# Kernel tuning notes

Measured on AMD Instinct MI355X. Metric: run time of the kernel, lower is better.

## Reference

```python
import jax, jax.numpy as jnp
import numpy as np

B, H, E = 1024, 2048, 1024

def _xavier(key, shape):
    # torch xavier_normal_ on [1, out, in]: std = sqrt(2/(fan_in+fan_out)) over last two dims
    fan_out, fan_in = shape[-2], shape[-1]
    std = (2.0 / (fan_in + fan_out)) ** 0.5
    return jax.random.normal(key, shape, jnp.float32) * std

def setup_inputs() -> dict:
    key = jax.random.key(0)
    ks = jax.random.split(key, 17)
    inp = {
        'x': jax.random.normal(ks[0], (B, E, 1), jnp.float32),
        'c': jax.random.normal(ks[1], (B, H, 1), jnp.float32),
        'h': jax.random.normal(ks[2], (B, H, 1), jnp.float32),
        'W_xi': _xavier(ks[3], (1, H, E)), 'W_hi': _xavier(ks[4], (1, H, H)), 'B_i': _xavier(ks[5], (1, H, 1)),
        'W_xg': _xavier(ks[6], (1, H, E)), 'W_hg': _xavier(ks[7], (1, H, H)), 'B_g': _xavier(ks[8], (1, H, 1)),
        'W_xf': _xavier(ks[9], (1, H, E)), 'W_hf': _xavier(ks[10], (1, H, H)), 'B_f': _xavier(ks[11], (1, H, 1)),
        'W_xo': _xavier(ks[12], (1, H, E)), 'W_ho': _xavier(ks[13], (1, H, H)), 'B_o': _xavier(ks[14], (1, H, 1)),
        'W_hy': _xavier(ks[15], (1, E, H)), 'B_y': _xavier(ks[16], (1, E, 1)),
    }
    return inp

def reference(x, c, h, W_xi, W_hi, B_i, W_xg, W_hg, B_g, W_xf, W_hf, B_f, W_xo, W_ho, B_o, W_hy, B_y):
    # jnp.matmul broadcasts the leading batch dim: [1,H,E] @ [B,E,1] -> [B,H,1]
    i = jax.nn.sigmoid(jnp.matmul(W_xi, x) + jnp.matmul(W_hi, h) + B_i)
    g = jnp.tanh(jnp.matmul(W_xg, x) + jnp.matmul(W_hg, h) + B_g)
    f = jax.nn.sigmoid(jnp.matmul(W_xf, x) + jnp.matmul(W_hf, h) + B_f)
    c_new = f * c + i * g
    o = jax.nn.sigmoid(jnp.matmul(W_xo, x) + jnp.matmul(W_ho, h) + B_o)
    h_new = o * c_new  # NOTE: source uses o*c (no tanh), faithful to original
    y = jnp.tanh(jnp.matmul(W_hy, h_new) + B_y)
    return (y, c_new, h_new)
```

## Files before the change

kernel.cpp:

```cpp
#include <hip/hip_runtime.h>

#define B_SZ 1024
#define H_SZ 2048
#define E_SZ 1024

typedef float  f32x4 __attribute__((ext_vector_type(4)));
typedef short  s16x8 __attribute__((ext_vector_type(8)));

__device__ __forceinline__ unsigned short f2bf(float f) {
    unsigned u = __float_as_uint(f);
    u = u + 0x7fffu + ((u >> 16) & 1u);
    return (unsigned short)(u >> 16);
}
__device__ __forceinline__ float bf2f(unsigned short s) {
    return __uint_as_float(((unsigned)s) << 16);
}
__device__ __forceinline__ float sigm(float v) {
    return 1.0f / (1.0f + __expf(-v));
}

__device__ __forceinline__ void gll(const unsigned short* g, unsigned short* l) {
    __builtin_amdgcn_global_load_lds(
        (const __attribute__((address_space(1))) unsigned int*)g,
        (__attribute__((address_space(3))) unsigned int*)l, 16, 0, 0);
}

struct CastArgs {
    const float*    src[11];
    unsigned short* dst[11];
    int             n[11];
};

__global__ __launch_bounds__(256) void cast_kernel(CastArgs a) {
    const int arr = blockIdx.y;
    const int n = a.n[arr];
    const float* __restrict__ s = a.src[arr];
    unsigned short* __restrict__ d = a.dst[arr];
    const int stride = gridDim.x * 256 * 4;
    for (int i = (blockIdx.x * 256 + threadIdx.x) * 4; i < n; i += stride) {
        float4 v = *(const float4*)(s + i);
        ushort4 o;
        o.x = f2bf(v.x); o.y = f2bf(v.y); o.z = f2bf(v.z); o.w = f2bf(v.w);
        *(ushort4*)(d + i) = o;
    }
}

__device__ __forceinline__ void gemm_accum64(
    const unsigned short* __restrict__ A,
    const unsigned short* __restrict__ W,
    int ld, int kLen, int m0, int n0,
    unsigned short* lA, unsigned short* lB,
    f32x4 acc[4][4], int t)
{
    const int lane = t & 63;
    const int w    = t >> 6;
    const int wr   = (w >> 1) << 6;
    const int wc   = (w & 1) << 6;
    const int lr   = lane & 15;
    const int q4   = lane >> 4;

    const int srow = t >> 3;
    const int scol = ((t & 7) ^ (srow & 7)) << 3;
    const unsigned short* gA = A + (size_t)(m0 + srow) * ld + scol;
    const unsigned short* gB = W + (size_t)(n0 + srow) * ld + scol;
    const size_t st32 = (size_t)32 * ld;

    const int cb0 = ((q4    ) ^ (lr & 7)) << 3;
    const int cb1 = ((4 + q4) ^ (lr & 7)) << 3;

    for (int k0 = 0; k0 < kLen; k0 += 64) {
#pragma unroll
        for (int p = 0; p < 4; ++p)
            gll(gA + k0 + p * st32, lA + (t + 256 * p) * 8);
#pragma unroll
        for (int p = 0; p < 4; ++p)
            gll(gB + k0 + p * st32, lB + (t + 256 * p) * 8);
        __syncthreads();

#pragma unroll
        for (int ks = 0; ks < 2; ++ks) {
            const int cb = ks ? cb1 : cb0;
            s16x8 af[4], bfr[4];
#pragma unroll
            for (int i = 0; i < 4; ++i)
                af[i] = *(const s16x8*)(lA + (wr + i * 16 + lr) * 64 + cb);
#pragma unroll
            for (int j = 0; j < 4; ++j)
                bfr[j] = *(const s16x8*)(lB + (wc + j * 16 + lr) * 64 + cb);
#pragma unroll
            for (int i = 0; i < 4; ++i)
#pragma unroll
                for (int j = 0; j < 4; ++j)
                    acc[i][j] = __builtin_amdgcn_mfma_f32_16x16x32_bf16(
                        af[i], bfr[j], acc[i][j], 0, 0, 0);
        }
        __syncthreads();
    }
}

__global__ __launch_bounds__(256) void gates_kernel(
    const unsigned short* __restrict__ Xb,
    const unsigned short* __restrict__ Hb,
    const unsigned short* __restrict__ Wxb,
    const unsigned short* __restrict__ Whb,
    const float* __restrict__ bi, const float* __restrict__ bg,
    const float* __restrict__ bff, const float* __restrict__ bo,
    unsigned short* __restrict__ Z)
{
    __shared__ unsigned short lA[128 * 64];
    __shared__ unsigned short lB[128 * 64];
    const int t   = threadIdx.x;
    const int b   = blockIdx.x;
    const int xcd = b & 7;
    const int i_  = b >> 3;
    const int nt  = xcd * 8 + (i_ >> 3);
    const int m0  = (i_ & 7) * 128;
    const int q   = nt >> 4;
    const int n0  = (nt & 15) * 128;

    f32x4 acc[4][4] = {};
    gemm_accum64(Xb, Wxb + (size_t)q * H_SZ * E_SZ, E_SZ, E_SZ, m0, n0, lA, lB, acc, t);
    gemm_accum64(Hb, Whb + (size_t)q * H_SZ * H_SZ, H_SZ, H_SZ, m0, n0, lA, lB, acc, t);

    const float* bias = (q == 0) ? bi : (q == 1) ? bg : (q == 2) ? bff : bo;
    const int lane = t & 63, w = t >> 6;
    const int wr = (w >> 1) << 6, wc = (w & 1) << 6;
    const int lr = lane & 15, rq = (lane >> 4) << 2;
    unsigned short* Zq = Z + (size_t)q * B_SZ * H_SZ;
#pragma unroll
    for (int i = 0; i < 4; ++i) {
#pragma unroll
        for (int j = 0; j < 4; ++j) {
            const int n = n0 + wc + j * 16 + lr;
            const float bv = bias[n];
#pragma unroll
            for (int r = 0; r < 4; ++r) {
                const int m = m0 + wr + i * 16 + rq + r;
                const float v = acc[i][j][r] + bv;
                const float a = (q == 1) ? tanhf(v) : sigm(v);
                Zq[(size_t)m * H_SZ + n] = f2bf(a);
            }
        }
    }
}

__global__ __launch_bounds__(256) void cell_kernel(
    const unsigned short* __restrict__ Z, const float* __restrict__ c,
    float* __restrict__ c_out, float* __restrict__ h_out,
    unsigned short* __restrict__ HnB)
{
    const size_t BH = (size_t)B_SZ * H_SZ;
    const int idx = (blockIdx.x * 256 + threadIdx.x) * 4;
    ushort4 iu = *(const ushort4*)(Z + idx);
    ushort4 gu = *(const ushort4*)(Z + BH + idx);
    ushort4 fu = *(const ushort4*)(Z + 2 * BH + idx);
    ushort4 ou = *(const ushort4*)(Z + 3 * BH + idx);
    float4 cv = *(const float4*)(c + idx);

    float cn[4], hn[4];
    cn[0] = bf2f(fu.x) * cv.x + bf2f(iu.x) * bf2f(gu.x);
    cn[1] = bf2f(fu.y) * cv.y + bf2f(iu.y) * bf2f(gu.y);
    cn[2] = bf2f(fu.z) * cv.z + bf2f(iu.z) * bf2f(gu.z);
    cn[3] = bf2f(fu.w) * cv.w + bf2f(iu.w) * bf2f(gu.w);
    hn[0] = bf2f(ou.x) * cn[0];
    hn[1] = bf2f(ou.y) * cn[1];
    hn[2] = bf2f(ou.z) * cn[2];
    hn[3] = bf2f(ou.w) * cn[3];

    *(float4*)(c_out + idx) = make_float4(cn[0], cn[1], cn[2], cn[3]);
    *(float4*)(h_out + idx) = make_float4(hn[0], hn[1], hn[2], hn[3]);
    ushort4 hb;
    hb.x = f2bf(hn[0]); hb.y = f2bf(hn[1]); hb.z = f2bf(hn[2]); hb.w = f2bf(hn[3]);
    *(ushort4*)(HnB + idx) = hb;
}

__global__ __launch_bounds__(256) void y_split_kernel(
    const unsigned short* __restrict__ Hn,
    const unsigned short* __restrict__ Wy,
    float* __restrict__ part)
{
    __shared__ unsigned short lA[128 * 64];
    __shared__ unsigned short lB[128 * 64];
    const int t   = threadIdx.x;
    const int b   = blockIdx.x;
    const int xcd = b & 7;
    const int i_  = b >> 3;
    const int ns  = xcd * 4 + (i_ >> 3);
    const int m0  = (i_ & 7) * 128;
    const int n0  = (ns >> 2) * 128;
    const int s   = ns & 3;

    f32x4 acc[4][4] = {};
    gemm_accum64(Hn + s * 512, Wy + s * 512, H_SZ, 512, m0, n0, lA, lB, acc, t);

    const int lane = t & 63, w = t >> 6;
    const int wr = (w >> 1) << 6, wc = (w & 1) << 6;
    const int lr = lane & 15, rq = (lane >> 4) << 2;
    float* P = part + (size_t)s * B_SZ * E_SZ;
#pragma unroll
    for (int i = 0; i < 4; ++i) {
#pragma unroll
        for (int j = 0; j < 4; ++j) {
            const int n = n0 + wc + j * 16 + lr;
#pragma unroll
            for (int r = 0; r < 4; ++r) {
                const int m = m0 + wr + i * 16 + rq + r;
                P[(size_t)m * E_SZ + n] = acc[i][j][r];
            }
        }
    }
}

__global__ __launch_bounds__(256) void y_reduce_kernel(
    const float* __restrict__ part, const float* __restrict__ by,
    float* __restrict__ yout)
{
    const size_t BE = (size_t)B_SZ * E_SZ;
    const int idx = (blockIdx.x * 256 + threadIdx.x) * 4;
    float4 a = *(const float4*)(part + idx);
    float4 b2 = *(const float4*)(part + BE + idx);
    float4 c2 = *(const float4*)(part + 2 * BE + idx);
    float4 d2 = *(const float4*)(part + 3 * BE + idx);
    const int col = idx & (E_SZ - 1);
    float4 bv = *(const float4*)(by + col);
    float4 o;
    o.x = tanhf(a.x + b2.x + c2.x + d2.x + bv.x);
    o.y = tanhf(a.y + b2.y + c2.y + d2.y + bv.y);
    o.z = tanhf(a.z + b2.z + c2.z + d2.z + bv.z);
    o.w = tanhf(a.w + b2.w + c2.w + d2.w + bv.w);
    *(float4*)(yout + idx) = o;
}

extern "C" void kernel_launch(void* const* d_in, const int* in_sizes, int n_in,
                              void* d_out, int out_size, void* d_ws, size_t ws_size,
                              hipStream_t stream) {
    const float* x   = (const float*)d_in[0];
    const float* c   = (const float*)d_in[1];
    const float* h   = (const float*)d_in[2];
    const float* Wxi = (const float*)d_in[3];
    const float* Whi = (const float*)d_in[4];
    const float* Bi  = (const float*)d_in[5];
    const float* Wxg = (const float*)d_in[6];
    const float* Whg = (const float*)d_in[7];
    const float* Bg  = (const float*)d_in[8];
    const float* Wxf = (const float*)d_in[9];
    const float* Whf = (const float*)d_in[10];
    const float* Bf  = (const float*)d_in[11];
    const float* Wxo = (const float*)d_in[12];
    const float* Who = (const float*)d_in[13];
    const float* Bo  = (const float*)d_in[14];
    const float* Why = (const float*)d_in[15];
    const float* By  = (const float*)d_in[16];

    const size_t BE = (size_t)B_SZ * E_SZ, BH = (size_t)B_SZ * H_SZ;
    const size_t HE = (size_t)H_SZ * E_SZ, HH = (size_t)H_SZ * H_SZ;
    const size_t EH = (size_t)E_SZ * H_SZ;

    unsigned short* ws   = (unsigned short*)d_ws;
    unsigned short* Xb   = ws;
    unsigned short* Hb   = Xb + BE;
    unsigned short* Wxb  = Hb + BH;
    unsigned short* Whb  = Wxb + 4 * HE;
    unsigned short* Whyb = Whb + 4 * HH;
    unsigned short* Z    = Whyb + EH;
    unsigned short* HnB  = Z + 4 * BH;

    CastArgs ca;
    ca.src[0]  = x;   ca.dst[0]  = Xb;           ca.n[0]  = (int)BE;
    ca.src[1]  = h;   ca.dst[1]  = Hb;           ca.n[1]  = (int)BH;
    ca.src[2]  = Wxi; ca.dst[2]  = Wxb;          ca.n[2]  = (int)HE;
    ca.src[3]  = Wxg; ca.dst[3]  = Wxb + HE;     ca.n[3]  = (int)HE;
    ca.src[4]  = Wxf; ca.dst[4]  = Wxb + 2 * HE; ca.n[4]  = (int)HE;
    ca.src[5]  = Wxo; ca.dst[5]  = Wxb + 3 * HE; ca.n[5]  = (int)HE;
    ca.src[6]  = Whi; ca.dst[6]  = Whb;          ca.n[6]  = (int)HH;
    ca.src[7]  = Whg; ca.dst[7]  = Whb + HH;     ca.n[7]  = (int)HH;
    ca.src[8]  = Whf; ca.dst[8]  = Whb + 2 * HH; ca.n[8]  = (int)HH;
    ca.src[9]  = Who; ca.dst[9]  = Whb + 3 * HH; ca.n[9]  = (int)HH;
    ca.src[10] = Why; ca.dst[10] = Whyb;         ca.n[10] = (int)EH;

    hipLaunchKernelGGL(cast_kernel, dim3(1024, 11), dim3(256), 0, stream, ca);
    hipLaunchKernelGGL(gates_kernel, dim3(512), dim3(256), 0, stream,
                       Xb, Hb, Wxb, Whb, Bi, Bg, Bf, Bo, Z);

    float* y_out = (float*)d_out;
    float* c_out = y_out + BE;
    float* h_out = c_out + BH;
    hipLaunchKernelGGL(cell_kernel, dim3((unsigned)(BH / 1024)), dim3(256), 0, stream,
                       Z, c, c_out, h_out, HnB);

    float* ypart = (float*)Z;
    hipLaunchKernelGGL(y_split_kernel, dim3(256), dim3(256), 0, stream,
                       HnB, Whyb, ypart);
    hipLaunchKernelGGL(y_reduce_kernel, dim3((unsigned)(BE / 1024)), dim3(256), 0, stream,
                       ypart, By, y_out);
}
```

Before: 267.0 us.

## Fuse all LSTM phases into one cooperative persistent kernel with grid syncs

Replaces five separate launches (cast, gates GEMM, cell, split-K y GEMM, reduce) with a single cooperative kernel of 256 blocks of 512 threads that separates the phases with grid.sync. A non-cooperative multi-kernel path is kept as a fallback. Each GEMM block now computes two 128x128 output tiles that share one A tile, and the y GEMM uses 8-way split-K with partials stored in the freed Wx buffer. The aim is to cut launch gaps and reuse A loads, at the cost of grid-sync overhead, fixed parallelism for the elementwise phases, and occupancy limits from 48KB of LDS per block.

```diff
diff --git a/kernel.cpp b/kernel.cpp
--- a/kernel.cpp
+++ b/kernel.cpp
@@ -1,8 +1,14 @@
 #include <hip/hip_runtime.h>
+#include <hip/hip_cooperative_groups.h>
+
+namespace cg = cooperative_groups;
 
 #define B_SZ 1024
 #define H_SZ 2048
 #define E_SZ 1024
+#define GRID 256
+#define BLK  512
+#define NTHR (GRID * BLK)
 
 typedef float  f32x4 __attribute__((ext_vector_type(4)));
 typedef short  s16x8 __attribute__((ext_vector_type(8)));
@@ -18,26 +24,26 @@
 __device__ __forceinline__ float sigm(float v) {
     return 1.0f / (1.0f + __expf(-v));
 }
-
 __device__ __forceinline__ void gll(const unsigned short* g, unsigned short* l) {
     __builtin_amdgcn_global_load_lds(
         (const __attribute__((address_space(1))) unsigned int*)g,
         (__attribute__((address_space(3))) unsigned int*)l, 16, 0, 0);
 }
 
-struct CastArgs {
-    const float*    src[11];
-    unsigned short* dst[11];
-    int             n[11];
+struct Params {
+    const float *x, *c, *h;
+    const float *Wxi, *Whi, *Bi, *Wxg, *Whg, *Bg;
+    const float *Wxf, *Whf, *Bf, *Wxo, *Who, *Bo;
+    const float *Why, *By;
+    unsigned short *Xb, *Hb, *Wxb, *Whb, *Whyb, *Z, *HnB;
+    float *ypart;
+    float *y_out, *c_out, *h_out;
 };
 
-__global__ __launch_bounds__(256) void cast_kernel(CastArgs a) {
-    const int arr = blockIdx.y;
-    const int n = a.n[arr];
-    const float* __restrict__ s = a.src[arr];
-    unsigned short* __restrict__ d = a.dst[arr];
-    const int stride = gridDim.x * 256 * 4;
-    for (int i = (blockIdx.x * 256 + threadIdx.x) * 4; i < n; i += stride) {
+__device__ __forceinline__ void cast_arr(const float* __restrict__ s,
+                                         unsigned short* __restrict__ d,
+                                         int n, int gtid) {
+    for (int i = gtid * 4; i < n; i += NTHR * 4) {
         float4 v = *(const float4*)(s + i);
         ushort4 o;
         o.x = f2bf(v.x); o.y = f2bf(v.y); o.z = f2bf(v.z); o.w = f2bf(v.w);
@@ -45,36 +51,57 @@
     }
 }
 
-__device__ __forceinline__ void gemm_accum64(
+__device__ __forceinline__ void ph_cast(const Params& p, int gtid) {
+    const int BE = B_SZ * E_SZ, BH = B_SZ * H_SZ;
+    const int HE = H_SZ * E_SZ, HH_ = 1 << 22;
+    cast_arr(p.x,   p.Xb,                 BE,  gtid);
+    cast_arr(p.h,   p.Hb,                 BH,  gtid);
+    cast_arr(p.Wxi, p.Wxb,                HE,  gtid);
+    cast_arr(p.Wxg, p.Wxb + (size_t)HE,   HE,  gtid);
+    cast_arr(p.Wxf, p.Wxb + 2*(size_t)HE, HE,  gtid);
+    cast_arr(p.Wxo, p.Wxb + 3*(size_t)HE, HE,  gtid);
+    cast_arr(p.Whi, p.Whb,                HH_, gtid);
+    cast_arr(p.Whg, p.Whb + (size_t)HH_,  HH_, gtid);
+    cast_arr(p.Whf, p.Whb + 2*(size_t)HH_,HH_, gtid);
+    cast_arr(p.Who, p.Whb + 3*(size_t)HH_,HH_, gtid);
+    cast_arr(p.Why, p.Whyb,               HE,  gtid);
+}
+
+__device__ __forceinline__ void gemm_dual(
     const unsigned short* __restrict__ A,
-    const unsigned short* __restrict__ W,
-    int ld, int kLen, int m0, int n0,
-    unsigned short* lA, unsigned short* lB,
+    const unsigned short* __restrict__ W0,
+    const unsigned short* __restrict__ W1,
+    int ld, int kLen, int m0, int nA, int nB,
+    unsigned short* lA, unsigned short* lB0, unsigned short* lB1,
     f32x4 acc[4][4], int t)
 {
     const int lane = t & 63;
     const int w    = t >> 6;
-    const int wr   = (w >> 1) << 6;
-    const int wc   = (w & 1) << 6;
+    const int g    = w >> 2;
+    const int wg   = w & 3;
+    const int wr   = (wg >> 1) << 6;
+    const int wc   = (wg & 1) << 6;
     const int lr   = lane & 15;
     const int q4   = lane >> 4;
 
     const int srow = t >> 3;
     const int scol = ((t & 7) ^ (srow & 7)) << 3;
-    const unsigned short* gA = A + (size_t)(m0 + srow) * ld + scol;
-    const unsigned short* gB = W + (size_t)(n0 + srow) * ld + scol;
-    const size_t st32 = (size_t)32 * ld;
+    const unsigned short* gA  = A  + (size_t)(m0 + srow) * ld + scol;
+    const unsigned short* gB0 = W0 + (size_t)(nA + srow) * ld + scol;
+    const unsigned short* gB1 = W1 + (size_t)(nB + srow) * ld + scol;
+    const size_t st64 = (size_t)64 * ld;
+    unsigned short* myB = g ? lB1 : lB0;
 
     const int cb0 = ((q4    ) ^ (lr & 7)) << 3;
     const int cb1 = ((4 + q4) ^ (lr & 7)) << 3;
 
     for (int k0 = 0; k0 < kLen; k0 += 64) {
-#pragma unroll
-        for (int p = 0; p < 4; ++p)
-            gll(gA + k0 + p * st32, lA + (t + 256 * p) * 8);
-#pragma unroll
-        for (int p = 0; p < 4; ++p)
-            gll(gB + k0 + p * st32, lB + (t + 256 * p) * 8);
+        gll(gA  + k0,        lA  + t * 8);
+        gll(gA  + k0 + st64, lA  + (t + 512) * 8);
+        gll(gB0 + k0,        lB0 + t * 8);
+        gll(gB0 + k0 + st64, lB0 + (t + 512) * 8);
+        gll(gB1 + k0,        lB1 + t * 8);
+        gll(gB1 + k0 + st64, lB1 + (t + 512) * 8);
         __syncthreads();
 
 #pragma unroll
@@ -86,7 +113,7 @@
                 af[i] = *(const s16x8*)(lA + (wr + i * 16 + lr) * 64 + cb);
 #pragma unroll
             for (int j = 0; j < 4; ++j)
-                bfr[j] = *(const s16x8*)(lB + (wc + j * 16 + lr) * 64 + cb);
+                bfr[j] = *(const s16x8*)(myB + (wc + j * 16 + lr) * 64 + cb);
 #pragma unroll
             for (int i = 0; i < 4; ++i)
 #pragma unroll
@@ -98,45 +125,43 @@
     }
 }
 
-__global__ __launch_bounds__(256) void gates_kernel(
-    const unsigned short* __restrict__ Xb,
-    const unsigned short* __restrict__ Hb,
-    const unsigned short* __restrict__ Wxb,
-    const unsigned short* __restrict__ Whb,
-    const float* __restrict__ bi, const float* __restrict__ bg,
-    const float* __restrict__ bff, const float* __restrict__ bo,
-    unsigned short* __restrict__ Z)
-{
-    __shared__ unsigned short lA[128 * 64];
-    __shared__ unsigned short lB[128 * 64];
-    const int t   = threadIdx.x;
-    const int b   = blockIdx.x;
-    const int xcd = b & 7;
-    const int i_  = b >> 3;
-    const int nt  = xcd * 8 + (i_ >> 3);
-    const int m0  = (i_ & 7) * 128;
-    const int q   = nt >> 4;
-    const int n0  = (nt & 15) * 128;
+__device__ __forceinline__ void ph_gates(const Params& p, int b, int t,
+                                         unsigned short* lA,
+                                         unsigned short* lB0,
+                                         unsigned short* lB1) {
+    const size_t HE = (size_t)H_SZ * E_SZ, HH = (size_t)H_SZ * H_SZ;
+    const size_t BH = (size_t)B_SZ * H_SZ;
+    const int xcd = b & 7, i_ = b >> 3;
+    const int j = i_ >> 3, mt = i_ & 7;
+    const int nt0 = xcd * 8 + j, nt1 = nt0 + 4;
+    const int q0 = nt0 >> 4, q1 = nt1 >> 4;
+    const int n00 = (nt0 & 15) * 128, n01 = (nt1 & 15) * 128;
+    const int m0 = mt * 128;
 
     f32x4 acc[4][4] = {};
-    gemm_accum64(Xb, Wxb + (size_t)q * H_SZ * E_SZ, E_SZ, E_SZ, m0, n0, lA, lB, acc, t);
-    gemm_accum64(Hb, Whb + (size_t)q * H_SZ * H_SZ, H_SZ, H_SZ, m0, n0, lA, lB, acc, t);
-
-    const float* bias = (q == 0) ? bi : (q == 1) ? bg : (q == 2) ? bff : bo;
+    gemm_dual(p.Xb, p.Wxb + (size_t)q0 * HE, p.Wxb + (size_t)q1 * HE,
+              E_SZ, E_SZ, m0, n00, n01, lA, lB0, lB1, acc, t);
+    gemm_dual(p.Hb, p.Whb + (size_t)q0 * HH, p.Whb + (size_t)q1 * HH,
+              H_SZ, H_SZ, m0, n00, n01, lA, lB0, lB1, acc, t);
+
     const int lane = t & 63, w = t >> 6;
-    const int wr = (w >> 1) << 6, wc = (w & 1) << 6;
+    const int g = w >> 2, wg = w & 3;
+    const int q = g ? q1 : q0;
+    const int n0 = g ? n01 : n00;
+    const float* bias = (q == 0) ? p.Bi : (q == 1) ? p.Bg : (q == 2) ? p.Bf : p.Bo;
+    const int wr = (wg >> 1) << 6, wc = (wg & 1) << 6;
     const int lr = lane & 15, rq = (lane >> 4) << 2;
-    unsigned short* Zq = Z + (size_t)q * B_SZ * H_SZ;
+    unsigned short* Zq = p.Z + (size_t)q * BH;
 #pragma unroll
     for (int i = 0; i < 4; ++i) {
 #pragma unroll
-        for (int j = 0; j < 4; ++j) {
-            const int n = n0 + wc + j * 16 + lr;
+        for (int jj = 0; jj < 4; ++jj) {
+            const int n = n0 + wc + jj * 16 + lr;
             const float bv = bias[n];
 #pragma unroll
             for (int r = 0; r < 4; ++r) {
                 const int m = m0 + wr + i * 16 + rq + r;
-                const float v = acc[i][j][r] + bv;
+                const float v = acc[i][jj][r] + bv;
                 const float a = (q == 1) ? tanhf(v) : sigm(v);
                 Zq[(size_t)m * H_SZ + n] = f2bf(a);
             }
@@ -144,153 +169,193 @@
     }
 }
 
-__global__ __launch_bounds__(256) void cell_kernel(
-    const unsigned short* __restrict__ Z, const float* __restrict__ c,
-    float* __restrict__ c_out, float* __restrict__ h_out,
-    unsigned short* __restrict__ HnB)
-{
+__device__ __forceinline__ void ph_cell(const Params& p, int gtid) {
     const size_t BH = (size_t)B_SZ * H_SZ;
-    const int idx = (blockIdx.x * 256 + threadIdx.x) * 4;
-    ushort4 iu = *(const ushort4*)(Z + idx);
-    ushort4 gu = *(const ushort4*)(Z + BH + idx);
-    ushort4 fu = *(const ushort4*)(Z + 2 * BH + idx);
-    ushort4 ou = *(const ushort4*)(Z + 3 * BH + idx);
-    float4 cv = *(const float4*)(c + idx);
-
-    float cn[4], hn[4];
-    cn[0] = bf2f(fu.x) * cv.x + bf2f(iu.x) * bf2f(gu.x);
-    cn[1] = bf2f(fu.y) * cv.y + bf2f(iu.y) * bf2f(gu.y);
-    cn[2] = bf2f(fu.z) * cv.z + bf2f(iu.z) * bf2f(gu.z);
-    cn[3] = bf2f(fu.w) * cv.w + bf2f(iu.w) * bf2f(gu.w);
-    hn[0] = bf2f(ou.x) * cn[0];
-    hn[1] = bf2f(ou.y) * cn[1];
-    hn[2] = bf2f(ou.z) * cn[2];
-    hn[3] = bf2f(ou.w) * cn[3];
-
-    *(float4*)(c_out + idx) = make_float4(cn[0], cn[1], cn[2], cn[3]);
-    *(float4*)(h_out + idx) = make_float4(hn[0], hn[1], hn[2], hn[3]);
-    ushort4 hb;
-    hb.x = f2bf(hn[0]); hb.y = f2bf(hn[1]); hb.z = f2bf(hn[2]); hb.w = f2bf(hn[3]);
-    *(ushort4*)(HnB + idx) = hb;
-}
-
-__global__ __launch_bounds__(256) void y_split_kernel(
-    const unsigned short* __restrict__ Hn,
-    const unsigned short* __restrict__ Wy,
-    float* __restrict__ part)
-{
-    __shared__ unsigned short lA[128 * 64];
-    __shared__ unsigned short lB[128 * 64];
-    const int t   = threadIdx.x;
-    const int b   = blockIdx.x;
-    const int xcd = b & 7;
-    const int i_  = b >> 3;
-    const int ns  = xcd * 4 + (i_ >> 3);
-    const int m0  = (i_ & 7) * 128;
-    const int n0  = (ns >> 2) * 128;
-    const int s   = ns & 3;
+    for (int idx = gtid * 4; idx < (int)BH; idx += NTHR * 4) {
+        ushort4 iu = *(const ushort4*)(p.Z + idx);
+        ushort4 gu = *(const ushort4*)(p.Z + BH + idx);
+        ushort4 fu = *(const ushort4*)(p.Z + 2 * BH + idx);
+        ushort4 ou = *(const ushort4*)(p.Z + 3 * BH + idx);
+        float4 cv = *(const float4*)(p.c + idx);
+
+        float cn[4], hn[4];
+        cn[0] = bf2f(fu.x) * cv.x + bf2f(iu.x) * bf2f(gu.x);
+        cn[1] = bf2f(fu.y) * cv.y + bf2f(iu.y) * bf2f(gu.y);
+        cn[2] = bf2f(fu.z) * cv.z + bf2f(iu.z) * bf2f(gu.z);
+        cn[3] = bf2f(fu.w) * cv.w + bf2f(iu.w) * bf2f(gu.w);
+        hn[0] = bf2f(ou.x) * cn[0];
+        hn[1] = bf2f(ou.y) * cn[1];
+        hn[2] = bf2f(ou.z) * cn[2];
+        hn[3] = bf2f(ou.w) * cn[3];
+
+        *(float4*)(p.c_out + idx) = make_float4(cn[0], cn[1], cn[2], cn[3]);
+        *(float4*)(p.h_out + idx) = make_float4(hn[0], hn[1], hn[2], hn[3]);
+        ushort4 hb;
+        hb.x = f2bf(hn[0]); hb.y = f2bf(hn[1]);
+        hb.z = f2bf(hn[2]); hb.w = f2bf(hn[3]);
+        *(ushort4*)(p.HnB + idx) = hb;
+    }
+}
+
+__device__ __forceinline__ void ph_y(const Params& p, int b, int t,
+                                     unsigned short* lA,
+                                     unsigned short* lB0,
+                                     unsigned short* lB1) {
+    const size_t BE = (size_t)B_SZ * E_SZ;
+    const int s = b >> 5, rem = b & 31;
+    const int np = rem >> 3, mt = rem & 7;
+    const int n00 = np * 128, n01 = (np + 4) * 128;
+    const int m0 = mt * 128;
+
+    const unsigned short* A = p.HnB  + s * 256;
+    const unsigned short* W = p.Whyb + s * 256;
 
     f32x4 acc[4][4] = {};
-    gemm_accum64(Hn + s * 512, Wy + s * 512, H_SZ, 512, m0, n0, lA, lB, acc, t);
+    gemm_dual(A, W, W, H_SZ, 256, m0, n00, n01, lA, lB0, lB1, acc, t);
 
     const int lane = t & 63, w = t >> 6;
-    const int wr = (w >> 1) << 6, wc = (w & 1) << 6;
+    const int g = w >> 2, wg = w & 3;
+    const int n0 = g ? n01 : n00;
+    const int wr = (wg >> 1) << 6, wc = (wg & 1) << 6;
     const int lr = lane & 15, rq = (lane >> 4) << 2;
-    float* P = part + (size_t)s * B_SZ * E_SZ;
+    float* P = p.ypart + (size_t)s * BE;
 #pragma unroll
     for (int i = 0; i < 4; ++i) {
 #pragma unroll
-        for (int j = 0; j < 4; ++j) {
-            const int n = n0 + wc + j * 16 + lr;
+        for (int jj = 0; jj < 4; ++jj) {
+            const int n = n0 + wc + jj * 16 + lr;
 #pragma unroll
             for (int r = 0; r < 4; ++r) {
                 const int m = m0 + wr + i * 16 + rq + r;
-                P[(size_t)m * E_SZ + n] = acc[i][j][r];
+                P[(size_t)m * E_SZ + n] = acc[i][jj][r];
             }
         }
     }
 }
 
-__global__ __launch_bounds__(256) void y_reduce_kernel(
-    const float* __restrict__ part, const float* __restrict__ by,
-    float* __restrict__ yout)
-{
+__device__ __forceinline__ void ph_reduce(const Params& p, int gtid) {
     const size_t BE = (size_t)B_SZ * E_SZ;
-    const int idx = (blockIdx.x * 256 + threadIdx.x) * 4;
-    float4 a = *(const float4*)(part + idx);
-    float4 b2 = *(const float4*)(part + BE + idx);
-    float4 c2 = *(const float4*)(part + 2 * BE + idx);
-    float4 d2 = *(const float4*)(part + 3 * BE + idx);
-    const int col = idx & (E_SZ - 1);
-    float4 bv = *(const float4*)(by + col);
-    float4 o;
-    o.x = tanhf(a.x + b2.x + c2.x + d2.x + bv.x);
-    o.y = tanhf(a.y + b2.y + c2.y + d2.y + bv.y);
-    o.z = tanhf(a.z + b2.z + c2.z + d2.z + bv.z);
-    o.w = tanhf(a.w + b2.w + c2.w + d2.w + bv.w);
-    *(float4*)(yout + idx) = o;
+    for (int idx = gtid * 4; idx < (int)BE; idx += NTHR * 4) {
+        float4 s0 = *(const float4*)(p.ypart + idx);
+#pragma unroll
+        for (int s = 1; s < 8; ++s) {
+            float4 ps = *(const float4*)(p.ypart + (size_t)s * BE + idx);
+            s0.x += ps.x; s0.y += ps.y; s0.z += ps.z; s0.w += ps.w;
+        }
+        const int col = idx & (E_SZ - 1);
+        float4 bv = *(const float4*)(p.By + col);
+        float4 o;
+        o.x = tanhf(s0.x + bv.x);
+        o.y = tanhf(s0.y + bv.y);
+        o.z = tanhf(s0.z + bv.z);
+        o.w = tanhf(s0.w + bv.w);
+        *(float4*)(p.y_out + idx) = o;
+    }
+}
+
+__global__ __launch_bounds__(BLK, 2) void lstm_mega(Params p) {
+    __shared__ unsigned short lA[128 * 64];
+    __shared__ unsigned short lB0[128 * 64];
+    __shared__ unsigned short lB1[128 * 64];
+    cg::grid_group grid = cg::this_grid();
+    const int t = threadIdx.x, b = blockIdx.x;
+    const int gtid = b * BLK + t;
+
+    ph_cast(p, gtid);
+    __threadfence(); grid.sync();
+    ph_gates(p, b, t, lA, lB0, lB1);
+    __threadfence(); grid.sync();
+    ph_cell(p, gtid);
+    __threadfence(); grid.sync();
+    ph_y(p, b, t, lA, lB0, lB1);
+    __threadfence(); grid.sync();
+    ph_reduce(p, gtid);
+}
+
+__global__ __launch_bounds__(BLK) void k_cast(Params p) {
+    ph_cast(p, blockIdx.x * BLK + threadIdx.x);
+}
+__global__ __launch_bounds__(BLK) void k_gates(Params p) {
+    __shared__ unsigned short lA[128 * 64];
+    __shared__ unsigned short lB0[128 * 64];
+    __shared__ unsigned short lB1[128 * 64];
+    ph_gates(p, blockIdx.x, threadIdx.x, lA, lB0, lB1);
+}
+__global__ __launch_bounds__(BLK) void k_cell(Params p) {
+    ph_cell(p, blockIdx.x * BLK + threadIdx.x);
+}
+__global__ __launch_bounds__(BLK) void k_y(Params p) {
+    __shared__ unsigned short lA[128 * 64];
+    __shared__ unsigned short lB0[128 * 64];
+    __shared__ unsigned short lB1[128 * 64];
+    ph_y(p, blockIdx.x, threadIdx.x, lA, lB0, lB1);
+}
+__global__ __launch_bounds__(BLK) void k_reduce(Params p) {
+    ph_reduce(p, blockIdx.x * BLK + threadIdx.x);
 }
 
 extern "C" void kernel_launch(void* const* d_in, const int* in_sizes, int n_in,
                               void* d_out, int out_size, void* d_ws, size_t ws_size,
                               hipStream_t stream) {
-    const float* x   = (const float*)d_in[0];
-    const float* c   = (const float*)d_in[1];
-    const float* h   = (const float*)d_in[2];
-    const float* Wxi = (const float*)d_in[3];
-    const float* Whi = (const float*)d_in[4];
-    const float* Bi  = (const float*)d_in[5];
-    const float* Wxg = (const float*)d_in[6];
-    const float* Whg = (const float*)d_in[7];
-    const float* Bg  = (const float*)d_in[8];
-    const float* Wxf = (const float*)d_in[9];
-    const float* Whf = (const float*)d_in[10];
-    const float* Bf  = (const float*)d_in[11];
-    const float* Wxo = (const float*)d_in[12];
-    const float* Who = (const float*)d_in[13];
-    const float* Bo  = (const float*)d_in[14];
-    const float* Why = (const float*)d_in[15];
-    const float* By  = (const float*)d_in[16];
-
     const size_t BE = (size_t)B_SZ * E_SZ, BH = (size_t)B_SZ * H_SZ;
     const size_t HE = (size_t)H_SZ * E_SZ, HH = (size_t)H_SZ * H_SZ;
     const size_t EH = (size_t)E_SZ * H_SZ;
 
-    unsigned short* ws   = (unsigned short*)d_ws;
-    unsigned short* Xb   = ws;
-    unsigned short* Hb   = Xb + BE;
-    unsigned short* Wxb  = Hb + BH;
-    unsigned short* Whb  = Wxb + 4 * HE;
-    unsigned short* Whyb = Whb + 4 * HH;
-    unsigned short* Z    = Whyb + EH;
-    unsigned short* HnB  = Z + 4 * BH;
-
-    CastArgs ca;
-    ca.src[0]  = x;   ca.dst[0]  = Xb;           ca.n[0]  = (int)BE;
-    ca.src[1]  = h;   ca.dst[1]  = Hb;           ca.n[1]  = (int)BH;
-    ca.src[2]  = Wxi; ca.dst[2]  = Wxb;          ca.n[2]  = (int)HE;
-    ca.src[3]  = Wxg; ca.dst[3]  = Wxb + HE;     ca.n[3]  = (int)HE;
-    ca.src[4]  = Wxf; ca.dst[4]  = Wxb + 2 * HE; ca.n[4]  = (int)HE;
-    ca.src[5]  = Wxo; ca.dst[5]  = Wxb + 3 * HE; ca.n[5]  = (int)HE;
-    ca.src[6]  = Whi; ca.dst[6]  = Whb;          ca.n[6]  = (int)HH;
-    ca.src[7]  = Whg; ca.dst[7]  = Whb + HH;     ca.n[7]  = (int)HH;
-    ca.src[8]  = Whf; ca.dst[8]  = Whb + 2 * HH; ca.n[8]  = (int)HH;
-    ca.src[9]  = Who; ca.dst[9]  = Whb + 3 * HH; ca.n[9]  = (int)HH;
-    ca.src[10] = Why; ca.dst[10] = Whyb;         ca.n[10] = (int)EH;
-
-    hipLaunchKernelGGL(cast_kernel, dim3(1024, 11), dim3(256), 0, stream, ca);
-    hipLaunchKernelGGL(gates_kernel, dim3(512), dim3(256), 0, stream,
-                       Xb, Hb, Wxb, Whb, Bi, Bg, Bf, Bo, Z);
+    unsigned short* ws = (unsigned short*)d_ws;
+
+    Params prm;
+    prm.x   = (const float*)d_in[0];
+    prm.c   = (const float*)d_in[1];
+    prm.h   = (const float*)d_in[2];
+    prm.Wxi = (const float*)d_in[3];
+    prm.Whi = (const float*)d_in[4];
+    prm.Bi  = (const float*)d_in[5];
+    prm.Wxg = (const float*)d_in[6];
+    prm.Whg = (const float*)d_in[7];
+    prm.Bg  = (const float*)d_in[8];
+    prm.Wxf = (const float*)d_in[9];
+    prm.Whf = (const float*)d_in[10];
+    prm.Bf  = (const float*)d_in[11];
+    prm.Wxo = (const float*)d_in[12];
+    prm.Who = (const float*)d_in[13];
+    prm.Bo  = (const float*)d_in[14];
+    prm.Why = (const float*)d_in[15];
+    prm.By  = (const float*)d_in[16];
+
+    prm.Xb   = ws;
+    prm.Hb   = prm.Xb + BE;
+    prm.Wxb  = prm.Hb + BH;
+    prm.Whb  = prm.Wxb + 4 * HE;
+    prm.Whyb = prm.Whb + 4 * HH;
+    prm.Z    = prm.Whyb + EH;
+    prm.HnB  = prm.Z + 4 * BH;
+    prm.ypart = (float*)prm.Wxb;
 
     float* y_out = (float*)d_out;
-    float* c_out = y_out + BE;
-    float* h_out = c_out + BH;
-    hipLaunchKernelGGL(cell_kernel, dim3((unsigned)(BH / 1024)), dim3(256), 0, stream,
-                       Z, c, c_out, h_out, HnB);
-
-    float* ypart = (float*)Z;
-    hipLaunchKernelGGL(y_split_kernel, dim3(256), dim3(256), 0, stream,
-                       HnB, Whyb, ypart);
-    hipLaunchKernelGGL(y_reduce_kernel, dim3((unsigned)(BE / 1024)), dim3(256), 0, stream,
-                       ypart, By, y_out);
-}
+    prm.y_out = y_out;
+    prm.c_out = y_out + BE;
+    prm.h_out = prm.c_out + BH;
+
+    int dev = 0;
+    hipGetDevice(&dev);
+    int coop_ok = 0;
+    hipDeviceGetAttribute(&coop_ok, hipDeviceAttributeCooperativeLaunch, dev);
+    int maxb = 0;
+    hipOccupancyMaxActiveBlocksPerMultiprocessor(&maxb, lstm_mega, BLK, 0);
+
+    bool done = false;
+    if (coop_ok && maxb >= 1) {
+        void* args[] = { (void*)&prm };
+        hipError_t e = hipLaunchCooperativeKernel((const void*)lstm_mega,
+                                                  dim3(GRID), dim3(BLK),
+                                                  args, 0, stream);
+        done = (e == hipSuccess);
+    }
+    if (!done) {
+        hipLaunchKernelGGL(k_cast,   dim3(GRID), dim3(BLK), 0, stream, prm);
+        hipLaunchKernelGGL(k_gates,  dim3(GRID), dim3(BLK), 0, stream, prm);
+        hipLaunchKernelGGL(k_cell,   dim3(GRID), dim3(BLK), 0, stream, prm);
+        hipLaunchKernelGGL(k_y,      dim3(GRID), dim3(BLK), 0, stream, prm);
+        hipLaunchKernelGGL(k_reduce, dim3(GRID), dim3(BLK), 0, stream, prm);
+    }
+}
```

Result: slower. 679.3 us (+154.4%).
